# Kernel optimization log

Measured on AMD Instinct MI355X. Metric: run time of the kernel, lower is better.

Reference implementation:

```python
import jax, jax.numpy as jnp
import numpy as np

N = 50000      # nodes
E = 800000     # edges
C = 64         # irrep multiplicity (num_features)
H = 64         # radial MLP hidden
M = 64         # readout MLP width (MLP_irreps = 64x0e)
AVG_NEIGH = 16.0
SQRT3 = 3.0 ** 0.5  # component-normalized l=1 spherical harmonic scale


def setup_inputs() -> dict:
    key = jax.random.key(0)
    ks = jax.random.split(key, 24)
    g = lambda k, s, sc=1.0: jax.random.normal(k, s, dtype=jnp.float32) * sc
    w = C ** -0.5
    return {
        "vectors": g(ks[0], (E, 3)),
        "lengths": jax.random.uniform(ks[1], (E, 1), dtype=jnp.float32) * 5.0 + 0.1,
        "node_feats": g(ks[2], (N, 4 * C)),
        "edge_feats": g(ks[3], (E, C)),
        "edge_index": jax.random.randint(ks[4], (2, E), 0, N, dtype=jnp.int32),
        # interaction block: per-irrep linear_up, radial MLP (5 CG paths), per-irrep linear_post
        "W_s_up": g(ks[5], (C, C), w),
        "W_v_up": g(ks[6], (C, C), w),
        "mlp_w1": g(ks[7], (C, H), w),
        "mlp_w2": g(ks[8], (H, 5 * C), H ** -0.5),
        "W_s_post": g(ks[9], (C, C), w),
        "W_v_post": g(ks[10], (C, C), w),
        # product basis (correlation = 3) channel-mixing weights
        "P_s1": g(ks[11], (C, C), w),
        "P_s2": g(ks[12], (C, C), w),
        "P_s3": g(ks[13], (C, C), w),
        "P_vv": g(ks[14], (C, C), w),
        "P_v1": g(ks[15], (C, C), w),
        "P_v2": g(ks[16], (C, C), w),
        "P_v3": g(ks[17], (C, C), w),
        # non-linear readout (MLP_irreps scalars + gated vector output)
        "R_w1": g(ks[18], (C, M), w),
        "R_w2": g(ks[19], (M, C), M ** -0.5),
        "R_gate": g(ks[20], (M, 1), M ** -0.5),
        "R_vmix": g(ks[21], (C,), w),
    }


def reference(vectors, lengths, node_feats, edge_feats, edge_index,
              W_s_up, W_v_up, mlp_w1, mlp_w2, W_s_post, W_v_post,
              P_s1, P_s2, P_s3, P_vv, P_v1, P_v2, P_v3,
              R_w1, R_w2, R_gate, R_vmix):
    # split node feats into 64x0e scalars and 64x1o vectors
    s = node_feats[:, :C]                       # [N,C]
    v = node_feats[:, C:].reshape(-1, C, 3)     # [N,C,3]
    # linear_up (per-irrep channel mixing)
    s = s @ W_s_up
    v = jnp.einsum('nci,ck->nki', v, W_v_up)
    snd, rcv = edge_index[0], edge_index[1]
    sj = s[snd]                                  # [E,C] gather
    vj = v[snd]                                  # [E,C,3] gather
    # spherical harmonics, normalize=True, component normalization: Y0=1, Y1=sqrt(3)*rhat
    rhat = vectors / (jnp.linalg.norm(vectors, axis=-1, keepdims=True) + 1e-12)
    Y1 = SQRT3 * rhat                            # [E,3]
    # radial weights for the 5 CG paths (0x0->0, 1x1->0, 0x1->1, 1x0->1, 1x1->1)
    h = jax.nn.silu(edge_feats @ mlp_w1)
    w = (h @ mlp_w2).reshape(-1, 5, C)           # [E,5,C]
    vdY = jnp.einsum('eci,ei->ec', vj, Y1)       # 1x1 -> 0 (dot)
    m_s = w[:, 0] * sj + w[:, 1] * vdY           # [E,C]
    m_v = ((w[:, 2] * sj)[:, :, None] * Y1[:, None, :]   # 0x1 -> 1
           + w[:, 3][:, :, None] * vj                     # 1x0 -> 1
           + w[:, 4][:, :, None] * jnp.cross(vj, Y1[:, None, :]))  # 1x1 -> 1
    # scatter-sum messages to receiver nodes, normalize by avg_num_neighbors
    a_s = jax.ops.segment_sum(m_s, rcv, num_segments=N) / AVG_NEIGH
    a_v = jax.ops.segment_sum(m_v, rcv, num_segments=N) / AVG_NEIGH
    a_s = a_s @ W_s_post
    a_v = jnp.einsum('nci,ck->nki', a_v, W_v_post)
    # equivariant product basis, correlation up to 3 (symmetric contractions)
    vv = jnp.sum(a_v * a_v, axis=-1)             # invariant v.v per channel
    ps = a_s @ P_s1 + (a_s * a_s) @ P_s2 + (a_s ** 3) @ P_s3 + vv @ P_vv
    pv = (jnp.einsum('nci,ck->nki', a_v, P_v1)
          + jnp.einsum('nci,ck->nki', a_s[:, :, None] * a_v, P_v2)
          + jnp.einsum('nci,ck->nki', (a_s * a_s)[:, :, None] * a_v, P_v3))
    node_feats_out = jnp.concatenate([ps, pv.reshape(-1, 3 * C)], axis=-1)  # [N,4C]
    # non-linear readout: scalar MLP + gated vector channel mix
    hr = jax.nn.silu(ps @ R_w1)
    out_s = hr @ R_w2                            # [N,C]   -> node_out[:, :-3]
    gate = jax.nn.silu(hr @ R_gate)              # [N,1]
    vec = jnp.einsum('nci,c->ni', pv, R_vmix) * gate  # [N,3] -> node_out[:, -3:]
    return (out_s, vec, node_feats_out)
```

## Files before the change

### kernel.cpp

```cpp
#include <hip/hip_runtime.h>
#include <math.h>

constexpr int Nn = 50000;
constexpr int Ee = 800000;
constexpr int VEC_OFF = Nn * 64;
constexpr int NF_OFF  = Nn * 67;

constexpr int NBLK = 196;
constexpr int NPAD = NBLK * 256;
constexpr int WSW_F32_OFF = 1000000;

constexpr size_t AS_OFF = 0;
constexpr size_t AV_OFF = 12800000;

typedef short  bf16x8 __attribute__((ext_vector_type(8)));
typedef float  f32x4  __attribute__((ext_vector_type(4)));

#define MFMA16(a, b, c) __builtin_amdgcn_mfma_f32_16x16x32_bf16(a, b, c, 0, 0, 0)

__device__ __forceinline__ float silu(float x) { return x / (1.f + __expf(-x)); }

__device__ __forceinline__ unsigned short bfhi_u(float x) {
    union { float f; unsigned u; } c; c.f = x; return (unsigned short)(c.u >> 16);
}
__device__ __forceinline__ float bftrunc_f(float x) {
    union { float f; unsigned u; } c; c.f = x; c.u &= 0xffff0000u; return c.f;
}
__device__ __forceinline__ void split8(const float* p, bf16x8& hi, bf16x8& lo) {
#pragma unroll
    for (int j = 0; j < 8; j++) {
        float x = p[j];
        hi[j] = (short)bfhi_u(x);
        lo[j] = (short)bfhi_u(x - bftrunc_f(x));
    }
}

__global__ __launch_bounds__(256) void k_hist(const int* __restrict__ rcv,
                                              unsigned* __restrict__ cnt) {
    int e = blockIdx.x * 256 + threadIdx.x;
    atomicAdd(&cnt[rcv[e]], 1u);
}

__global__ __launch_bounds__(256) void k_scan_local(const unsigned* __restrict__ cnt,
                                                    unsigned* __restrict__ offs,
                                                    unsigned* __restrict__ bsum) {
    __shared__ unsigned s[256];
    int t = threadIdx.x, i = blockIdx.x * 256 + t;
    unsigned v = cnt[i];
    s[t] = v; __syncthreads();
    for (int d = 1; d < 256; d <<= 1) {
        unsigned x = (t >= d) ? s[t - d] : 0u; __syncthreads();
        s[t] += x; __syncthreads();
    }
    offs[i] = s[t] - v;
    if (t == 255) bsum[blockIdx.x] = s[255];
}

__global__ __launch_bounds__(256) void k_scan_bsum(unsigned* __restrict__ bsum) {
    __shared__ unsigned s[256];
    int t = threadIdx.x;
    unsigned v = (t < NBLK) ? bsum[t] : 0u;
    s[t] = v; __syncthreads();
    for (int d = 1; d < 256; d <<= 1) {
        unsigned x = (t >= d) ? s[t - d] : 0u; __syncthreads();
        s[t] += x; __syncthreads();
    }
    if (t < NBLK) bsum[t] = s[t] - v;
}

__global__ __launch_bounds__(256) void k_scan_add(unsigned* __restrict__ offs,
                                                  const unsigned* __restrict__ bsum) {
    int i = blockIdx.x * 256 + threadIdx.x;
    offs[i] += bsum[blockIdx.x];
}

__global__ __launch_bounds__(256) void k_scatter(const int* __restrict__ rcv,
                                                 unsigned* __restrict__ cursor,
                                                 unsigned* __restrict__ perm) {
    int e = blockIdx.x * 256 + threadIdx.x;
    unsigned p = atomicAdd(&cursor[rcv[e]], 1u);
    perm[p] = (unsigned)e;
}

__global__ __launch_bounds__(256) void k_wprep(const float* __restrict__ W1,
                                               const float* __restrict__ W2,
                                               unsigned short* __restrict__ wsw) {
    int t = blockIdx.x * 256 + threadIdx.x;
    int lane = t & 63;
    int ks = (t >> 6) & 1;
    int idx = t >> 7;
    int nt_all = idx % 24;
    int q2 = idx / 24;
    int g = lane >> 4, l15 = lane & 15;

    unsigned short* dst;
    float vals[8];
    if (nt_all < 4) {
        int n = nt_all * 16 + l15;
#pragma unroll
        for (int j = 0; j < 8; j++) {
            int k = ks * 32 + g * 8 + j;
            vals[j] = W1[k * 64 + n];
        }
        dst = wsw + (size_t)(((q2 * 4 + nt_all) * 2 + ks) * 64 + lane) * 8;
    } else {
        int nt = nt_all - 4;
        int n = nt * 16 + l15;
#pragma unroll
        for (int j = 0; j < 8; j++) {
            int k = ks * 32 + g * 8 + j;
            vals[j] = W2[k * 320 + n];
        }
        dst = wsw + 8192 + (size_t)(((q2 * 20 + nt) * 2 + ks) * 64 + lane) * 8;
    }
    bf16x8 o;
#pragma unroll
    for (int j = 0; j < 8; j++) {
        float x = vals[j];
        o[j] = q2 ? (short)bfhi_u(x - bftrunc_f(x)) : (short)bfhi_u(x);
    }
    *(bf16x8*)dst = o;
}

__global__ __launch_bounds__(256) void k_up(
    const float* __restrict__ nfeat,
    const float* __restrict__ Wsu, const float* __restrict__ Wvu,
    float4* __restrict__ up4) {
    __shared__ float sR[4][8][256];

    const int tid = threadIdx.x, lane = tid & 63, w = tid >> 6;
    const int nb = blockIdx.x * 32 + w * 8;

#pragma unroll
    for (int nn = 0; nn < 8; nn++) {
        int n = nb + nn;
        float4 nv = make_float4(0.f, 0.f, 0.f, 0.f);
        if (n < Nn) nv = *(const float4*)(nfeat + (size_t)n * 256 + lane * 4);
        *(float4*)(&sR[w][nn][lane * 4]) = nv;
    }

    float su[8], v0[8], v1[8], v2[8];
#pragma unroll
    for (int nn = 0; nn < 8; nn++) { su[nn]=0.f; v0[nn]=0.f; v1[nn]=0.f; v2[nn]=0.f; }

#pragma unroll 2
    for (int c = 0; c < 64; c++) {
        float u = Wsu[c * 64 + lane];
        float q = Wvu[c * 64 + lane];
#pragma unroll
        for (int nn = 0; nn < 8; nn++) {
            float sc = sR[w][nn][c];
            float a0 = sR[w][nn][64 + 3 * c + 0];
            float a1 = sR[w][nn][64 + 3 * c + 1];
            float a2 = sR[w][nn][64 + 3 * c + 2];
            su[nn] += sc * u;
            v0[nn] += a0 * q;
            v1[nn] += a1 * q;
            v2[nn] += a2 * q;
        }
    }
#pragma unroll
    for (int nn = 0; nn < 8; nn++) {
        int n = nb + nn;
        if (n < Nn)
            up4[(size_t)n * 64 + lane] = make_float4(su[nn], v0[nn], v1[nn], v2[nn]);
    }
}

__global__ __launch_bounds__(256, 3) void k_edge(
    const float* __restrict__ vectors, const float* __restrict__ edge_feats,
    const int* __restrict__ snd_idx, const int* __restrict__ rcv_idx,
    const unsigned* __restrict__ perm,
    const float4* __restrict__ up4,
    const unsigned short* __restrict__ wsw,
    float* __restrict__ a_s, float* __restrict__ a_v) {
    __shared__ float sU[5184];
    __shared__ float sH[64 * 68];
    __shared__ float sY[64 * 3];
    __shared__ int sSnd[64], sRcv[64];

    const int tid = threadIdx.x;
    const int e0 = blockIdx.x * 64;
    const int lane = tid & 63, w = tid >> 6, g = lane >> 4, l15 = lane & 15;

    if (tid < 64) {
        unsigned pe = perm[e0 + tid];
        float x = vectors[(size_t)pe * 3 + 0];
        float y = vectors[(size_t)pe * 3 + 1];
        float z = vectors[(size_t)pe * 3 + 2];
        float n = sqrtf(x * x + y * y + z * z) + 1e-12f;
        float s = 1.7320508075688772f / n;
        sY[tid * 3 + 0] = x * s; sY[tid * 3 + 1] = y * s; sY[tid * 3 + 2] = z * s;
        sSnd[tid] = snd_idx[pe];
        sRcv[tid] = rcv_idx[pe];
    }
    for (int kk = tid; kk < 1024; kk += 256) {
        int row = kk >> 4, part = kk & 15;
        unsigned pe = perm[e0 + row];
        *(f32x4*)(&sU[row * 68 + part * 4]) =
            *(const f32x4*)(edge_feats + (size_t)pe * 64 + part * 4);
    }
    __syncthreads();

    const bf16x8* W1f = (const bf16x8*)wsw;
    const bf16x8* W2f = (const bf16x8*)(wsw + 8192);

    {
        const f32x4 z4 = {0.f, 0.f, 0.f, 0.f};
        f32x4 acc1[4] = {z4, z4, z4, z4};
        bf16x8 b1h[2], b1l[2];
#pragma unroll
        for (int ks = 0; ks < 2; ks++) {
            b1h[ks] = W1f[((0 * 4 + w) * 2 + ks) * 64 + lane];
            b1l[ks] = W1f[((1 * 4 + w) * 2 + ks) * 64 + lane];
        }
#pragma unroll
        for (int mt = 0; mt < 4; mt++) {
#pragma unroll
            for (int ks = 0; ks < 2; ks++) {
                bf16x8 ah, al;
                split8(&sU[(mt * 16 + l15) * 68 + ks * 32 + 8 * g], ah, al);
                acc1[mt] = MFMA16(ah, b1h[ks], acc1[mt]);
                acc1[mt] = MFMA16(ah, b1l[ks], acc1[mt]);
                acc1[mt] = MFMA16(al, b1h[ks], acc1[mt]);
            }
        }
#pragma unroll
        for (int mt = 0; mt < 4; mt++)
#pragma unroll
            for (int i = 0; i < 4; i++)
                sH[(mt * 16 + g * 4 + i) * 68 + w * 16 + l15] = silu(acc1[mt][i]);
    }
    __syncthreads();

    for (int mt = 0; mt < 4; mt++) {
        bf16x8 a2h[2], a2l[2];
#pragma unroll
        for (int ks = 0; ks < 2; ks++)
            split8(&sH[(mt * 16 + l15) * 68 + ks * 32 + 8 * g], a2h[ks], a2l[ks]);

#pragma unroll
        for (int q = 0; q < 5; q++) {
            int nt = w * 5 + q;
            f32x4 acc = {0.f, 0.f, 0.f, 0.f};
#pragma unroll
            for (int ks = 0; ks < 2; ks++) {
                bf16x8 bh = W2f[((0 * 20 + nt) * 2 + ks) * 64 + lane];
                bf16x8 bl = W2f[((1 * 20 + nt) * 2 + ks) * 64 + lane];
                acc = MFMA16(a2h[ks], bh, acc);
                acc = MFMA16(a2h[ks], bl, acc);
                acc = MFMA16(a2l[ks], bh, acc);
            }
#pragma unroll
            for (int i = 0; i < 4; i++)
                sU[(g * 4 + i) * 324 + nt * 16 + l15] = acc[i];
        }
        __syncthreads();

        float4 gg[4];
#pragma unroll
        for (int t = 0; t < 4; t++)
            gg[t] = up4[(size_t)sSnd[mt * 16 + w * 4 + t] * 64 + lane];

        int curR = __builtin_amdgcn_readfirstlane(sRcv[mt * 16 + w * 4]);
        float accS = 0.f, aV0 = 0.f, aV1 = 0.f, aV2 = 0.f;
#pragma unroll
        for (int t = 0; t < 4; t++) {
            const int le = w * 4 + t, eb = mt * 16 + le;
            const int rcv = __builtin_amdgcn_readfirstlane(sRcv[eb]);
            const float w0 = sU[le * 324 + 0 * 64 + lane];
            const float w1 = sU[le * 324 + 1 * 64 + lane];
            const float w2 = sU[le * 324 + 2 * 64 + lane];
            const float w3 = sU[le * 324 + 3 * 64 + lane];
            const float w4 = sU[le * 324 + 4 * 64 + lane];
            const float Y0 = sY[eb * 3 + 0];
            const float Y1 = sY[eb * 3 + 1];
            const float Y2 = sY[eb * 3 + 2];
            const float sj = gg[t].x, vj0 = gg[t].y, vj1 = gg[t].z, vj2 = gg[t].w;
            float vdY = vj0 * Y0 + vj1 * Y1 + vj2 * Y2;
            float ms = w0 * sj + w1 * vdY;
            float cx = vj1 * Y2 - vj2 * Y1;
            float cy = vj2 * Y0 - vj0 * Y2;
            float cz = vj0 * Y1 - vj1 * Y0;
            float tt = w2 * sj;
            float mv0 = tt * Y0 + w3 * vj0 + w4 * cx;
            float mv1 = tt * Y1 + w3 * vj1 + w4 * cy;
            float mv2 = tt * Y2 + w3 * vj2 + w4 * cz;
            if (rcv != curR) {
                atomicAdd(a_s + (size_t)curR * 64 + lane, accS);
                float* avp = a_v + (size_t)curR * 192;
                atomicAdd(avp + lane,       aV0);
                atomicAdd(avp + 64 + lane,  aV1);
                atomicAdd(avp + 128 + lane, aV2);
                curR = rcv;
                accS = ms; aV0 = mv0; aV1 = mv1; aV2 = mv2;
            } else {
                accS += ms; aV0 += mv0; aV1 += mv1; aV2 += mv2;
            }
        }
        atomicAdd(a_s + (size_t)curR * 64 + lane, accS);
        {
            float* avp = a_v + (size_t)curR * 192;
            atomicAdd(avp + lane,       aV0);
            atomicAdd(avp + 64 + lane,  aV1);
            atomicAdd(avp + 128 + lane, aV2);
        }
        __syncthreads();
    }
}

__global__ __launch_bounds__(256) void k_post(
    const float* __restrict__ a_s, const float* __restrict__ a_v,
    const float* __restrict__ Wsp, const float* __restrict__ Wvp,
    const float* __restrict__ Ps1, const float* __restrict__ Ps2,
    const float* __restrict__ Ps3, const float* __restrict__ Pvv,
    const float* __restrict__ Pv1, const float* __restrict__ Pv2,
    const float* __restrict__ Pv3,
    const float* __restrict__ Rw1, const float* __restrict__ Rw2,
    const float* __restrict__ Rgate, const float* __restrict__ Rvmix,
    float* __restrict__ out) {
    __shared__ float Xb[4][8 * 256];
    __shared__ float Yb[4][8 * 256];

    const int tid = threadIdx.x, lane = tid & 63, w = tid >> 6;
    const int nb = blockIdx.x * 32 + w * 8;
    float* X = &Xb[w][0];
    float* Y = &Yb[w][0];

#pragma unroll
    for (int nn = 0; nn < 8; nn++) {
        int n = nb + nn;
        if (n < Nn) {
            X[nn * 256 + lane]       = a_s[(size_t)n * 64 + lane] * 0.0625f;
            X[nn * 256 + 64 + lane]  = a_v[(size_t)n * 192 + lane] * 0.0625f;
            X[nn * 256 + 128 + lane] = a_v[(size_t)n * 192 + 64 + lane] * 0.0625f;
            X[nn * 256 + 192 + lane] = a_v[(size_t)n * 192 + 128 + lane] * 0.0625f;
        } else {
            X[nn * 256 + lane] = 0.f; X[nn * 256 + 64 + lane] = 0.f;
            X[nn * 256 + 128 + lane] = 0.f; X[nn * 256 + 192 + lane] = 0.f;
        }
    }

    {
        float as2[8], ava[8], avb[8], avc[8];
#pragma unroll
        for (int nn = 0; nn < 8; nn++) { as2[nn]=0.f; ava[nn]=0.f; avb[nn]=0.f; avc[nn]=0.f; }
        for (int c = 0; c < 64; c++) {
            float wsp = Wsp[c * 64 + lane];
            float wvp = Wvp[c * 64 + lane];
#pragma unroll
            for (int nn = 0; nn < 8; nn++) {
                as2[nn] += X[nn * 256 + c] * wsp;
                ava[nn] += X[nn * 256 + 64 + c] * wvp;
                avb[nn] += X[nn * 256 + 128 + c] * wvp;
                avc[nn] += X[nn * 256 + 192 + c] * wvp;
            }
        }
#pragma unroll
        for (int nn = 0; nn < 8; nn++) {
            X[nn * 256 + lane] = as2[nn];
            X[nn * 256 + 64 + lane] = ava[nn];
            X[nn * 256 + 128 + lane] = avb[nn];
            X[nn * 256 + 192 + lane] = avc[nn];
        }
    }

    {
        float ps[8], pv0[8], pv1[8], pv2[8];
#pragma unroll
        for (int nn = 0; nn < 8; nn++) { ps[nn]=0.f; pv0[nn]=0.f; pv1[nn]=0.f; pv2[nn]=0.f; }
        for (int c = 0; c < 64; c++) {
            float p1 = Ps1[c * 64 + lane], p2 = Ps2[c * 64 + lane],
                  p3 = Ps3[c * 64 + lane], pv = Pvv[c * 64 + lane];
            float q1 = Pv1[c * 64 + lane], q2 = Pv2[c * 64 + lane],
                  q3 = Pv3[c * 64 + lane];
#pragma unroll
            for (int nn = 0; nn < 8; nn++) {
                float a  = X[nn * 256 + c];
                float b0 = X[nn * 256 + 64 + c];
                float b1 = X[nn * 256 + 128 + c];
                float b2 = X[nn * 256 + 192 + c];
                float a2 = a * a, a3 = a2 * a;
                float vv = b0 * b0 + b1 * b1 + b2 * b2;
                ps[nn] += a * p1 + a2 * p2 + a3 * p3 + vv * pv;
                float qq = q1 + a * q2 + a2 * q3;
                pv0[nn] += b0 * qq; pv1[nn] += b1 * qq; pv2[nn] += b2 * qq;
            }
        }
#pragma unroll
        for (int nn = 0; nn < 8; nn++) {
            Y[nn * 256 + lane] = ps[nn];
            Y[nn * 256 + 64 + lane] = pv0[nn];
            Y[nn * 256 + 128 + lane] = pv1[nn];
            Y[nn * 256 + 192 + lane] = pv2[nn];
            int n = nb + nn;
            if (n < Nn) {
                float* nf = out + NF_OFF + (size_t)n * 256;
                nf[lane] = ps[nn];
                nf[64 + lane * 3 + 0] = pv0[nn];
                nf[64 + lane * 3 + 1] = pv1[nn];
                nf[64 + lane * 3 + 2] = pv2[nn];
            }
        }
    }

    {
        float hr[8];
#pragma unroll
        for (int nn = 0; nn < 8; nn++) hr[nn] = 0.f;
        for (int c = 0; c < 64; c++) {
            float r1 = Rw1[c * 64 + lane];
#pragma unroll
            for (int nn = 0; nn < 8; nn++) hr[nn] += Y[nn * 256 + c] * r1;
        }
#pragma unroll
        for (int nn = 0; nn < 8; nn++) X[nn * 256 + lane] = silu(hr[nn]);
    }

    float gate[8];
    {
        float rg = Rgate[lane];
#pragma unroll
        for (int nn = 0; nn < 8; nn++) {
            float p = X[nn * 256 + lane] * rg;
            p += __shfl_xor(p, 1);  p += __shfl_xor(p, 2);
            p += __shfl_xor(p, 4);  p += __shfl_xor(p, 8);
            p += __shfl_xor(p, 16); p += __shfl_xor(p, 32);
            gate[nn] = silu(p);
        }
    }

    {
        float os[8];
#pragma unroll
        for (int nn = 0; nn < 8; nn++) os[nn] = 0.f;
        for (int c = 0; c < 64; c++) {
            float r2 = Rw2[c * 64 + lane];
#pragma unroll
            for (int nn = 0; nn < 8; nn++) os[nn] += X[nn * 256 + c] * r2;
        }
#pragma unroll
        for (int nn = 0; nn < 8; nn++) {
            int n = nb + nn;
            if (n < Nn) out[(size_t)n * 64 + lane] = os[nn];
        }
    }

    {
        float vm = Rvmix[lane];
#pragma unroll
        for (int nn = 0; nn < 8; nn++) {
            int n = nb + nn;
#pragma unroll
            for (int j = 0; j < 3; j++) {
                float p = Y[nn * 256 + 64 + j * 64 + lane] * vm;
                p += __shfl_xor(p, 1);  p += __shfl_xor(p, 2);
                p += __shfl_xor(p, 4);  p += __shfl_xor(p, 8);
                p += __shfl_xor(p, 16); p += __shfl_xor(p, 32);
                if (lane == j && n < Nn)
                    out[VEC_OFF + (size_t)n * 3 + j] = p * gate[nn];
            }
        }
    }
}

extern "C" void kernel_launch(void* const* d_in, const int* in_sizes, int n_in,
                              void* d_out, int out_size, void* d_ws, size_t ws_size,
                              hipStream_t stream) {
    (void)in_sizes; (void)n_in; (void)out_size; (void)ws_size;
    const float* vectors    = (const float*)d_in[0];
    const float* node_feats = (const float*)d_in[2];
    const float* edge_feats = (const float*)d_in[3];
    const int*   edge_index = (const int*)d_in[4];
    const float* W_s_up   = (const float*)d_in[5];
    const float* W_v_up   = (const float*)d_in[6];
    const float* mlp_w1   = (const float*)d_in[7];
    const float* mlp_w2   = (const float*)d_in[8];
    const float* W_s_post = (const float*)d_in[9];
    const float* W_v_post = (const float*)d_in[10];
    const float* P_s1 = (const float*)d_in[11];
    const float* P_s2 = (const float*)d_in[12];
    const float* P_s3 = (const float*)d_in[13];
    const float* P_vv = (const float*)d_in[14];
    const float* P_v1 = (const float*)d_in[15];
    const float* P_v2 = (const float*)d_in[16];
    const float* P_v3 = (const float*)d_in[17];
    const float* R_w1 = (const float*)d_in[18];
    const float* R_w2 = (const float*)d_in[19];
    const float* R_gate = (const float*)d_in[20];
    const float* R_vmix = (const float*)d_in[21];

    char* ws = (char*)d_ws;
    float* a_s = (float*)(ws + AS_OFF);
    float* a_v = (float*)(ws + AV_OFF);
    float* outp = (float*)d_out;
    unsigned* cnt  = (unsigned*)outp;
    unsigned* offs = cnt + NPAD;
    unsigned* bsum = offs + NPAD;
    unsigned* perm = bsum + 256;
    unsigned short* wsw = (unsigned short*)(outp + WSW_F32_OFF);
    float4* up4 = (float4*)(outp + NF_OFF);

    const int* snd = edge_index;
    const int* rcv = edge_index + Ee;

    hipMemsetAsync(ws, 0, 51200000, stream);
    hipMemsetAsync(cnt, 0, NPAD * sizeof(unsigned), stream);

    k_hist      <<<Ee / 256, 256, 0, stream>>>(rcv, cnt);
    k_scan_local<<<NBLK,     256, 0, stream>>>(cnt, offs, bsum);
    k_scan_bsum <<<1,        256, 0, stream>>>(bsum);
    k_scan_add  <<<NBLK,     256, 0, stream>>>(offs, bsum);
    k_scatter   <<<Ee / 256, 256, 0, stream>>>(rcv, offs, perm);

    k_wprep<<<24, 256, 0, stream>>>(mlp_w1, mlp_w2, wsw);
    k_up<<<(Nn + 31) / 32, 256, 0, stream>>>(node_feats, W_s_up, W_v_up, up4);

    k_edge<<<Ee / 64, 256, 0, stream>>>(vectors, edge_feats, snd, rcv,
                                        perm, up4, wsw, a_s, a_v);

    k_post<<<(Nn + 31) / 32, 256, 0, stream>>>(a_s, a_v,
                                               W_s_post, W_v_post,
                                               P_s1, P_s2, P_s3, P_vv,
                                               P_v1, P_v2, P_v3,
                                               R_w1, R_w2, R_gate, R_vmix,
                                               outp);
}
```

Before: 1.111 ms.

## Move post-aggregation node kernel matmuls onto split-bf16 MFMA

Rewrites k_post so every channel-mixing matmul (post linear, product basis, readout MLP) runs on 16x16x32 bf16 MFMA using a hi/lo split (three MFMAs per tile) instead of scalar FMA loops, with each wave now handling 16 nodes. Weight fragments are built directly from fp32 global weights per use. The bf16 splitting also switches from truncation to round-to-nearest-even everywhere, including the edge kernel and weight prep. This targets the FMA-bound node stage, at the cost of many repeated global weight loads and conversions per fragment, plus some precision change from the 3-term split.

```diff
diff --git a/kernel.cpp b/kernel.cpp
--- a/kernel.cpp
+++ b/kernel.cpp
@@ -20,19 +20,31 @@
 
 __device__ __forceinline__ float silu(float x) { return x / (1.f + __expf(-x)); }
 
-__device__ __forceinline__ unsigned short bfhi_u(float x) {
-    union { float f; unsigned u; } c; c.f = x; return (unsigned short)(c.u >> 16);
-}
-__device__ __forceinline__ float bftrunc_f(float x) {
-    union { float f; unsigned u; } c; c.f = x; c.u &= 0xffff0000u; return c.f;
-}
-__device__ __forceinline__ void split8(const float* p, bf16x8& hi, bf16x8& lo) {
-#pragma unroll
-    for (int j = 0; j < 8; j++) {
-        float x = p[j];
-        hi[j] = (short)bfhi_u(x);
-        lo[j] = (short)bfhi_u(x - bftrunc_f(x));
-    }
+__device__ __forceinline__ void rne_split(float x, short& h, short& l) {
+    union { float f; unsigned u; } c; c.f = x;
+    unsigned r = c.u + 0x7fffu + ((c.u >> 16) & 1u);
+    h = (short)(r >> 16);
+    union { float f; unsigned u; } hf; hf.u = (r >> 16) << 16;
+    union { float f; unsigned u; } d; d.f = x - hf.f;
+    unsigned r2 = d.u + 0x7fffu + ((d.u >> 16) & 1u);
+    l = (short)(r2 >> 16);
+}
+__device__ __forceinline__ void afrag(const float* v, bf16x8& hi, bf16x8& lo) {
+#pragma unroll
+    for (int j = 0; j < 8; j++) { short h, l; rne_split(v[j], h, l); hi[j] = h; lo[j] = l; }
+}
+__device__ __forceinline__ void bfrag(const float* __restrict__ W, int ldn,
+                                      int nt, int ks, int g, int l15,
+                                      bf16x8& bh, bf16x8& bl) {
+    const float* p = W + (size_t)(ks * 32 + 8 * g) * ldn + nt * 16 + l15;
+#pragma unroll
+    for (int j = 0; j < 8; j++) { short h, l; rne_split(p[(size_t)j * ldn], h, l); bh[j] = h; bl[j] = l; }
+}
+__device__ __forceinline__ f32x4 mm3(bf16x8 ah, bf16x8 al, bf16x8 bh, bf16x8 bl, f32x4 c) {
+    c = MFMA16(ah, bh, c);
+    c = MFMA16(ah, bl, c);
+    c = MFMA16(al, bh, c);
+    return c;
 }
 
 __global__ __launch_bounds__(256) void k_hist(const int* __restrict__ rcv,
@@ -98,26 +110,20 @@
     if (nt_all < 4) {
         int n = nt_all * 16 + l15;
 #pragma unroll
-        for (int j = 0; j < 8; j++) {
-            int k = ks * 32 + g * 8 + j;
-            vals[j] = W1[k * 64 + n];
-        }
+        for (int j = 0; j < 8; j++) vals[j] = W1[(ks * 32 + g * 8 + j) * 64 + n];
         dst = wsw + (size_t)(((q2 * 4 + nt_all) * 2 + ks) * 64 + lane) * 8;
     } else {
         int nt = nt_all - 4;
         int n = nt * 16 + l15;
 #pragma unroll
-        for (int j = 0; j < 8; j++) {
-            int k = ks * 32 + g * 8 + j;
-            vals[j] = W2[k * 320 + n];
-        }
+        for (int j = 0; j < 8; j++) vals[j] = W2[(ks * 32 + g * 8 + j) * 320 + n];
         dst = wsw + 8192 + (size_t)(((q2 * 20 + nt) * 2 + ks) * 64 + lane) * 8;
     }
     bf16x8 o;
 #pragma unroll
     for (int j = 0; j < 8; j++) {
-        float x = vals[j];
-        o[j] = q2 ? (short)bfhi_u(x - bftrunc_f(x)) : (short)bfhi_u(x);
+        short h, l; rne_split(vals[j], h, l);
+        o[j] = q2 ? l : h;
     }
     *(bf16x8*)dst = o;
 }
@@ -219,10 +225,8 @@
 #pragma unroll
             for (int ks = 0; ks < 2; ks++) {
                 bf16x8 ah, al;
-                split8(&sU[(mt * 16 + l15) * 68 + ks * 32 + 8 * g], ah, al);
-                acc1[mt] = MFMA16(ah, b1h[ks], acc1[mt]);
-                acc1[mt] = MFMA16(ah, b1l[ks], acc1[mt]);
-                acc1[mt] = MFMA16(al, b1h[ks], acc1[mt]);
+                afrag(&sU[(mt * 16 + l15) * 68 + ks * 32 + 8 * g], ah, al);
+                acc1[mt] = mm3(ah, al, b1h[ks], b1l[ks], acc1[mt]);
             }
         }
 #pragma unroll
@@ -237,7 +241,7 @@
         bf16x8 a2h[2], a2l[2];
 #pragma unroll
         for (int ks = 0; ks < 2; ks++)
-            split8(&sH[(mt * 16 + l15) * 68 + ks * 32 + 8 * g], a2h[ks], a2l[ks]);
+            afrag(&sH[(mt * 16 + l15) * 68 + ks * 32 + 8 * g], a2h[ks], a2l[ks]);
 
 #pragma unroll
         for (int q = 0; q < 5; q++) {
@@ -247,9 +251,7 @@
             for (int ks = 0; ks < 2; ks++) {
                 bf16x8 bh = W2f[((0 * 20 + nt) * 2 + ks) * 64 + lane];
                 bf16x8 bl = W2f[((1 * 20 + nt) * 2 + ks) * 64 + lane];
-                acc = MFMA16(a2h[ks], bh, acc);
-                acc = MFMA16(a2h[ks], bl, acc);
-                acc = MFMA16(a2l[ks], bh, acc);
+                acc = mm3(a2h[ks], a2l[ks], bh, bl, acc);
             }
 #pragma unroll
             for (int i = 0; i < 4; i++)
@@ -319,147 +321,234 @@
     const float* __restrict__ Rw1, const float* __restrict__ Rw2,
     const float* __restrict__ Rgate, const float* __restrict__ Rvmix,
     float* __restrict__ out) {
-    __shared__ float Xb[4][8 * 256];
-    __shared__ float Yb[4][8 * 256];
+    __shared__ float sQ[4][4][16 * 68];
 
     const int tid = threadIdx.x, lane = tid & 63, w = tid >> 6;
-    const int nb = blockIdx.x * 32 + w * 8;
-    float* X = &Xb[w][0];
-    float* Y = &Yb[w][0];
-
-#pragma unroll
-    for (int nn = 0; nn < 8; nn++) {
-        int n = nb + nn;
+    const int g = lane >> 4, l15 = lane & 15;
+    const int nb16 = blockIdx.x * 64 + w * 16;
+    float* q0 = &sQ[w][0][0];
+    float* q1 = &sQ[w][1][0];
+    float* q2 = &sQ[w][2][0];
+    float* q3 = &sQ[w][3][0];
+    const f32x4 z4 = {0.f, 0.f, 0.f, 0.f};
+    const int aoff0 = l15 * 68 + 8 * g;
+
+#pragma unroll 4
+    for (int nn = 0; nn < 16; nn++) {
+        int n = nb16 + nn;
+        float va = 0.f, vb = 0.f, vc = 0.f, vd = 0.f;
         if (n < Nn) {
-            X[nn * 256 + lane]       = a_s[(size_t)n * 64 + lane] * 0.0625f;
-            X[nn * 256 + 64 + lane]  = a_v[(size_t)n * 192 + lane] * 0.0625f;
-            X[nn * 256 + 128 + lane] = a_v[(size_t)n * 192 + 64 + lane] * 0.0625f;
-            X[nn * 256 + 192 + lane] = a_v[(size_t)n * 192 + 128 + lane] * 0.0625f;
-        } else {
-            X[nn * 256 + lane] = 0.f; X[nn * 256 + 64 + lane] = 0.f;
-            X[nn * 256 + 128 + lane] = 0.f; X[nn * 256 + 192 + lane] = 0.f;
-        }
+            va = a_s[(size_t)n * 64 + lane] * 0.0625f;
+            vb = a_v[(size_t)n * 192 + lane] * 0.0625f;
+            vc = a_v[(size_t)n * 192 + 64 + lane] * 0.0625f;
+            vd = a_v[(size_t)n * 192 + 128 + lane] * 0.0625f;
+        }
+        q0[nn * 68 + lane] = va; q1[nn * 68 + lane] = vb;
+        q2[nn * 68 + lane] = vc; q3[nn * 68 + lane] = vd;
     }
 
     {
-        float as2[8], ava[8], avb[8], avc[8];
-#pragma unroll
-        for (int nn = 0; nn < 8; nn++) { as2[nn]=0.f; ava[nn]=0.f; avb[nn]=0.f; avc[nn]=0.f; }
-        for (int c = 0; c < 64; c++) {
-            float wsp = Wsp[c * 64 + lane];
-            float wvp = Wvp[c * 64 + lane];
-#pragma unroll
-            for (int nn = 0; nn < 8; nn++) {
-                as2[nn] += X[nn * 256 + c] * wsp;
-                ava[nn] += X[nn * 256 + 64 + c] * wvp;
-                avb[nn] += X[nn * 256 + 128 + c] * wvp;
-                avc[nn] += X[nn * 256 + 192 + c] * wvp;
+        f32x4 aC[4] = {z4, z4, z4, z4}, b0C[4] = {z4, z4, z4, z4},
+              b1C[4] = {z4, z4, z4, z4}, b2C[4] = {z4, z4, z4, z4};
+#pragma unroll
+        for (int ks = 0; ks < 2; ks++) {
+            bf16x8 Ah[4], Al[4];
+            afrag(&q0[aoff0 + ks * 32], Ah[0], Al[0]);
+            afrag(&q1[aoff0 + ks * 32], Ah[1], Al[1]);
+            afrag(&q2[aoff0 + ks * 32], Ah[2], Al[2]);
+            afrag(&q3[aoff0 + ks * 32], Ah[3], Al[3]);
+#pragma unroll
+            for (int nt = 0; nt < 4; nt++) {
+                bf16x8 bh, bl;
+                bfrag(Wsp, 64, nt, ks, g, l15, bh, bl);
+                aC[nt] = mm3(Ah[0], Al[0], bh, bl, aC[nt]);
+                bfrag(Wvp, 64, nt, ks, g, l15, bh, bl);
+                b0C[nt] = mm3(Ah[1], Al[1], bh, bl, b0C[nt]);
+                b1C[nt] = mm3(Ah[2], Al[2], bh, bl, b1C[nt]);
+                b2C[nt] = mm3(Ah[3], Al[3], bh, bl, b2C[nt]);
             }
         }
 #pragma unroll
-        for (int nn = 0; nn < 8; nn++) {
-            X[nn * 256 + lane] = as2[nn];
-            X[nn * 256 + 64 + lane] = ava[nn];
-            X[nn * 256 + 128 + lane] = avb[nn];
-            X[nn * 256 + 192 + lane] = avc[nn];
-        }
-    }
-
-    {
-        float ps[8], pv0[8], pv1[8], pv2[8];
-#pragma unroll
-        for (int nn = 0; nn < 8; nn++) { ps[nn]=0.f; pv0[nn]=0.f; pv1[nn]=0.f; pv2[nn]=0.f; }
-        for (int c = 0; c < 64; c++) {
-            float p1 = Ps1[c * 64 + lane], p2 = Ps2[c * 64 + lane],
-                  p3 = Ps3[c * 64 + lane], pv = Pvv[c * 64 + lane];
-            float q1 = Pv1[c * 64 + lane], q2 = Pv2[c * 64 + lane],
-                  q3 = Pv3[c * 64 + lane];
-#pragma unroll
-            for (int nn = 0; nn < 8; nn++) {
-                float a  = X[nn * 256 + c];
-                float b0 = X[nn * 256 + 64 + c];
-                float b1 = X[nn * 256 + 128 + c];
-                float b2 = X[nn * 256 + 192 + c];
-                float a2 = a * a, a3 = a2 * a;
-                float vv = b0 * b0 + b1 * b1 + b2 * b2;
-                ps[nn] += a * p1 + a2 * p2 + a3 * p3 + vv * pv;
-                float qq = q1 + a * q2 + a2 * q3;
-                pv0[nn] += b0 * qq; pv1[nn] += b1 * qq; pv2[nn] += b2 * qq;
+        for (int nt = 0; nt < 4; nt++)
+#pragma unroll
+            for (int i = 0; i < 4; i++) {
+                int r = (g * 4 + i) * 68 + nt * 16 + l15;
+                q0[r] = aC[nt][i];  q1[r] = b0C[nt][i];
+                q2[r] = b1C[nt][i]; q3[r] = b2C[nt][i];
             }
-        }
-#pragma unroll
-        for (int nn = 0; nn < 8; nn++) {
-            Y[nn * 256 + lane] = ps[nn];
-            Y[nn * 256 + 64 + lane] = pv0[nn];
-            Y[nn * 256 + 128 + lane] = pv1[nn];
-            Y[nn * 256 + 192 + lane] = pv2[nn];
-            int n = nb + nn;
+    }
+
+    float aFv[2][8];
+#pragma unroll
+    for (int ks = 0; ks < 2; ks++)
+#pragma unroll
+        for (int j = 0; j < 8; j++) aFv[ks][j] = q0[aoff0 + ks * 32 + j];
+
+    f32x4 psC[4] = {z4, z4, z4, z4};
+    f32x4 pv0C[4] = {z4, z4, z4, z4}, pv1C[4] = {z4, z4, z4, z4},
+          pv2C[4] = {z4, z4, z4, z4};
+
+#pragma unroll
+    for (int ks = 0; ks < 2; ks++) {
+        float v2[8], v3[8], vv[8];
+#pragma unroll
+        for (int j = 0; j < 8; j++) {
+            float a = aFv[ks][j];
+            v2[j] = a * a; v3[j] = v2[j] * a;
+            float b0 = q1[aoff0 + ks * 32 + j];
+            float b1 = q2[aoff0 + ks * 32 + j];
+            float b2 = q3[aoff0 + ks * 32 + j];
+            vv[j] = b0 * b0 + b1 * b1 + b2 * b2;
+        }
+        bf16x8 A1h, A1l, A2h, A2l, A3h, A3l, AVh, AVl;
+        afrag(aFv[ks], A1h, A1l); afrag(v2, A2h, A2l);
+        afrag(v3, A3h, A3l);      afrag(vv, AVh, AVl);
+#pragma unroll
+        for (int nt = 0; nt < 4; nt++) {
+            bf16x8 bh, bl;
+            bfrag(Ps1, 64, nt, ks, g, l15, bh, bl); psC[nt] = mm3(A1h, A1l, bh, bl, psC[nt]);
+            bfrag(Ps2, 64, nt, ks, g, l15, bh, bl); psC[nt] = mm3(A2h, A2l, bh, bl, psC[nt]);
+            bfrag(Ps3, 64, nt, ks, g, l15, bh, bl); psC[nt] = mm3(A3h, A3l, bh, bl, psC[nt]);
+            bfrag(Pvv, 64, nt, ks, g, l15, bh, bl); psC[nt] = mm3(AVh, AVl, bh, bl, psC[nt]);
+        }
+    }
+#pragma unroll
+    for (int nt = 0; nt < 4; nt++)
+#pragma unroll
+        for (int i = 0; i < 4; i++) {
+            int r = g * 4 + i, n = nb16 + r;
+            q0[r * 68 + nt * 16 + l15] = psC[nt][i];
+            if (n < Nn)
+                out[NF_OFF + (size_t)n * 256 + nt * 16 + l15] = psC[nt][i];
+        }
+
+#pragma unroll
+    for (int ks = 0; ks < 2; ks++) {
+        bf16x8 Bh[9], Bl[9];
+#pragma unroll
+        for (int i3 = 0; i3 < 3; i3++) {
+            const float* qi = (i3 == 0) ? q1 : ((i3 == 1) ? q2 : q3);
+            float bF[8], ab[8], a2b[8];
+#pragma unroll
+            for (int j = 0; j < 8; j++) {
+                float b = qi[aoff0 + ks * 32 + j], a = aFv[ks][j];
+                bF[j] = b; ab[j] = a * b; a2b[j] = a * a * b;
+            }
+            afrag(bF,  Bh[i3 * 3 + 0], Bl[i3 * 3 + 0]);
+            afrag(ab,  Bh[i3 * 3 + 1], Bl[i3 * 3 + 1]);
+            afrag(a2b, Bh[i3 * 3 + 2], Bl[i3 * 3 + 2]);
+        }
+#pragma unroll
+        for (int nt = 0; nt < 4; nt++) {
+            bf16x8 p1h, p1l, p2h, p2l, p3h, p3l;
+            bfrag(Pv1, 64, nt, ks, g, l15, p1h, p1l);
+            bfrag(Pv2, 64, nt, ks, g, l15, p2h, p2l);
+            bfrag(Pv3, 64, nt, ks, g, l15, p3h, p3l);
+            pv0C[nt] = mm3(Bh[0], Bl[0], p1h, p1l, pv0C[nt]);
+            pv0C[nt] = mm3(Bh[1], Bl[1], p2h, p2l, pv0C[nt]);
+            pv0C[nt] = mm3(Bh[2], Bl[2], p3h, p3l, pv0C[nt]);
+            pv1C[nt] = mm3(Bh[3], Bl[3], p1h, p1l, pv1C[nt]);
+            pv1C[nt] = mm3(Bh[4], Bl[4], p2h, p2l, pv1C[nt]);
+            pv1C[nt] = mm3(Bh[5], Bl[5], p3h, p3l, pv1C[nt]);
+            pv2C[nt] = mm3(Bh[6], Bl[6], p1h, p1l, pv2C[nt]);
+            pv2C[nt] = mm3(Bh[7], Bl[7], p2h, p2l, pv2C[nt]);
+            pv2C[nt] = mm3(Bh[8], Bl[8], p3h, p3l, pv2C[nt]);
+        }
+    }
+#pragma unroll
+    for (int nt = 0; nt < 4; nt++)
+#pragma unroll
+        for (int i = 0; i < 4; i++) {
+            int n = nb16 + g * 4 + i;
             if (n < Nn) {
-                float* nf = out + NF_OFF + (size_t)n * 256;
-                nf[lane] = ps[nn];
-                nf[64 + lane * 3 + 0] = pv0[nn];
-                nf[64 + lane * 3 + 1] = pv1[nn];
-                nf[64 + lane * 3 + 2] = pv2[nn];
+                float* nf = out + NF_OFF + (size_t)n * 256 + 64;
+                int c = nt * 16 + l15;
+                nf[c * 3 + 0] = pv0C[nt][i];
+                nf[c * 3 + 1] = pv1C[nt][i];
+                nf[c * 3 + 2] = pv2C[nt][i];
             }
         }
-    }
-
-    {
-        float hr[8];
-#pragma unroll
-        for (int nn = 0; nn < 8; nn++) hr[nn] = 0.f;
-        for (int c = 0; c < 64; c++) {
-            float r1 = Rw1[c * 64 + lane];
-#pragma unroll
-            for (int nn = 0; nn < 8; nn++) hr[nn] += Y[nn * 256 + c] * r1;
-        }
-#pragma unroll
-        for (int nn = 0; nn < 8; nn++) X[nn * 256 + lane] = silu(hr[nn]);
-    }
-
-    float gate[8];
-    {
-        float rg = Rgate[lane];
-#pragma unroll
-        for (int nn = 0; nn < 8; nn++) {
-            float p = X[nn * 256 + lane] * rg;
-            p += __shfl_xor(p, 1);  p += __shfl_xor(p, 2);
-            p += __shfl_xor(p, 4);  p += __shfl_xor(p, 8);
-            p += __shfl_xor(p, 16); p += __shfl_xor(p, 32);
-            gate[nn] = silu(p);
-        }
-    }
-
-    {
-        float os[8];
-#pragma unroll
-        for (int nn = 0; nn < 8; nn++) os[nn] = 0.f;
-        for (int c = 0; c < 64; c++) {
-            float r2 = Rw2[c * 64 + lane];
-#pragma unroll
-            for (int nn = 0; nn < 8; nn++) os[nn] += X[nn * 256 + c] * r2;
-        }
-#pragma unroll
-        for (int nn = 0; nn < 8; nn++) {
-            int n = nb + nn;
-            if (n < Nn) out[(size_t)n * 64 + lane] = os[nn];
-        }
-    }
-
-    {
-        float vm = Rvmix[lane];
-#pragma unroll
-        for (int nn = 0; nn < 8; nn++) {
-            int n = nb + nn;
-#pragma unroll
-            for (int j = 0; j < 3; j++) {
-                float p = Y[nn * 256 + 64 + j * 64 + lane] * vm;
-                p += __shfl_xor(p, 1);  p += __shfl_xor(p, 2);
-                p += __shfl_xor(p, 4);  p += __shfl_xor(p, 8);
-                p += __shfl_xor(p, 16); p += __shfl_xor(p, 32);
-                if (lane == j && n < Nn)
-                    out[VEC_OFF + (size_t)n * 3 + j] = p * gate[nn];
-            }
+
+    f32x4 hrC[4] = {z4, z4, z4, z4};
+#pragma unroll
+    for (int ks = 0; ks < 2; ks++) {
+        bf16x8 ah, al;
+        afrag(&q0[aoff0 + ks * 32], ah, al);
+#pragma unroll
+        for (int nt = 0; nt < 4; nt++) {
+            bf16x8 bh, bl;
+            bfrag(Rw1, 64, nt, ks, g, l15, bh, bl);
+            hrC[nt] = mm3(ah, al, bh, bl, hrC[nt]);
+        }
+    }
+#pragma unroll
+    for (int nt = 0; nt < 4; nt++)
+#pragma unroll
+        for (int i = 0; i < 4; i++) hrC[nt][i] = silu(hrC[nt][i]);
+
+    float rg[4], gate4[4];
+#pragma unroll
+    for (int nt = 0; nt < 4; nt++) rg[nt] = Rgate[nt * 16 + l15];
+#pragma unroll
+    for (int ii = 0; ii < 4; ii++) {
+        float p = hrC[0][ii] * rg[0] + hrC[1][ii] * rg[1] +
+                  hrC[2][ii] * rg[2] + hrC[3][ii] * rg[3];
+        p += __shfl_xor(p, 1); p += __shfl_xor(p, 2);
+        p += __shfl_xor(p, 4); p += __shfl_xor(p, 8);
+        gate4[ii] = silu(p);
+    }
+#pragma unroll
+    for (int nt = 0; nt < 4; nt++)
+#pragma unroll
+        for (int i = 0; i < 4; i++)
+            q1[(g * 4 + i) * 68 + nt * 16 + l15] = hrC[nt][i];
+
+    f32x4 osC[4] = {z4, z4, z4, z4};
+#pragma unroll
+    for (int ks = 0; ks < 2; ks++) {
+        bf16x8 ah, al;
+        afrag(&q1[aoff0 + ks * 32], ah, al);
+#pragma unroll
+        for (int nt = 0; nt < 4; nt++) {
+            bf16x8 bh, bl;
+            bfrag(Rw2, 64, nt, ks, g, l15, bh, bl);
+            osC[nt] = mm3(ah, al, bh, bl, osC[nt]);
+        }
+    }
+#pragma unroll
+    for (int nt = 0; nt < 4; nt++)
+#pragma unroll
+        for (int i = 0; i < 4; i++) {
+            int n = nb16 + g * 4 + i;
+            if (n < Nn) out[(size_t)n * 64 + nt * 16 + l15] = osC[nt][i];
+        }
+
+    float vm[4];
+#pragma unroll
+    for (int nt = 0; nt < 4; nt++) vm[nt] = Rvmix[nt * 16 + l15];
+#pragma unroll
+    for (int ii = 0; ii < 4; ii++) {
+        int n = nb16 + g * 4 + ii;
+        {
+            float p = pv0C[0][ii] * vm[0] + pv0C[1][ii] * vm[1] +
+                      pv0C[2][ii] * vm[2] + pv0C[3][ii] * vm[3];
+            p += __shfl_xor(p, 1); p += __shfl_xor(p, 2);
+            p += __shfl_xor(p, 4); p += __shfl_xor(p, 8);
+            if (l15 == 0 && n < Nn) out[VEC_OFF + (size_t)n * 3 + 0] = p * gate4[ii];
+        }
+        {
+            float p = pv1C[0][ii] * vm[0] + pv1C[1][ii] * vm[1] +
+                      pv1C[2][ii] * vm[2] + pv1C[3][ii] * vm[3];
+            p += __shfl_xor(p, 1); p += __shfl_xor(p, 2);
+            p += __shfl_xor(p, 4); p += __shfl_xor(p, 8);
+            if (l15 == 1 && n < Nn) out[VEC_OFF + (size_t)n * 3 + 1] = p * gate4[ii];
+        }
+        {
+            float p = pv2C[0][ii] * vm[0] + pv2C[1][ii] * vm[1] +
+                      pv2C[2][ii] * vm[2] + pv2C[3][ii] * vm[3];
+            p += __shfl_xor(p, 1); p += __shfl_xor(p, 2);
+            p += __shfl_xor(p, 4); p += __shfl_xor(p, 8);
+            if (l15 == 2 && n < Nn) out[VEC_OFF + (size_t)n * 3 + 2] = p * gate4[ii];
         }
     }
 }
@@ -519,7 +608,7 @@
     k_edge<<<Ee / 64, 256, 0, stream>>>(vectors, edge_feats, snd, rcv,
                                         perm, up4, wsw, a_s, a_v);
 
-    k_post<<<(Nn + 31) / 32, 256, 0, stream>>>(a_s, a_v,
+    k_post<<<(Nn + 63) / 64, 256, 0, stream>>>(a_s, a_v,
                                                W_s_post, W_v_post,
                                                P_s1, P_s2, P_s3, P_vv,
                                                P_v1, P_v2, P_v3,
```

Result: faster. 975.7 us (-12.2%).
